# Kernel tuning notes

Measured on AMD Instinct MI355X. Metric: run time of the kernel, lower is better.

## Reference

```python
import jax, jax.numpy as jnp
import numpy as np
import math

E = 8        # num_experts
L2 = 15
L3 = 32
D = 3072     # eval_features_per_perspective
R = 256      # router_features
B = 16384
AUX_ALPHA = 0.01
Z_ALPHA = 0.001


def setup_inputs() -> dict:
    key = jax.random.key(0)
    ks = jax.random.split(key, 12)
    inp = {
        "expert_input": jax.random.uniform(ks[0], (B, D), jnp.float32),
        "router_input": jax.random.normal(ks[1], (R,) , jnp.float32) * 0 + jax.random.normal(ks[1], (B, R), jnp.float32),
        # router init: normal(std=0.01), zero bias (as in _reset_router)
        "router_w": jax.random.normal(ks[2], (E, R), jnp.float32) * 0.01,
        "router_b": jnp.zeros((E,), jnp.float32),
        # FactorizedStackedLinear l1: stacked weight [E*(L2+1), D] + shared factorized [(L2+1), D]
        "l1_w": jax.random.normal(ks[3], (E * (L2 + 1), D), jnp.float32) * (1.0 / math.sqrt(D)),
        "l1_b": jax.random.normal(ks[4], (E * (L2 + 1),), jnp.float32) * 0.01,
        "l1f_w": jax.random.normal(ks[5], (L2 + 1, D), jnp.float32) * (1.0 / math.sqrt(D)),
        "l1f_b": jax.random.normal(ks[6], (L2 + 1,), jnp.float32) * 0.01,
        # StackedLinear l2: [E*L3, 2*L2]
        "l2_w": jax.random.normal(ks[7], (E * L3, 2 * L2), jnp.float32) * (1.0 / math.sqrt(2 * L2)),
        "l2_b": jax.random.normal(ks[8], (E * L3,), jnp.float32) * 0.01,
        # StackedLinear output: [E*1, L3], bias zeroed in __init__
        "out_w": jax.random.normal(ks[9], (E, L3), jnp.float32) * (1.0 / math.sqrt(L3)),
        "out_b": jnp.zeros((E,), jnp.float32),
    }
    return inp


def reference(expert_input, router_input, router_w, router_b,
              l1_w, l1_b, l1f_w, l1f_b, l2_w, l2_b, out_w, out_b):
    # ---- router + straight-through hard gate ----
    gate_logits = router_input @ router_w.T + router_b                      # [B, E]
    gate_probs = jax.nn.softmax(gate_logits, axis=-1)
    expert_indices = jnp.argmax(gate_logits, axis=-1)                       # [B]
    hard_gate = jax.nn.one_hot(expert_indices, E, dtype=gate_probs.dtype)   # [B, E]
    gate = hard_gate + gate_probs - jax.lax.stop_gradient(gate_probs)

    # ---- routing metrics / losses ----
    fraction_routed = hard_gate.mean(axis=0)                                 # [E]
    avg_gate_prob = gate_probs.mean(axis=0)                                  # [E]
    aux_loss = E * jnp.sum(fraction_routed * avg_gate_prob)
    z_loss = jnp.mean(jnp.square(jax.nn.logsumexp(gate_logits, axis=-1)))
    entropy = jnp.mean(-jnp.sum(gate_probs * jnp.log(jnp.clip(gate_probs, 1e-9)), axis=-1))
    normalized_entropy = entropy / jnp.float32(math.log(max(E, 2)))
    top1_prob = jnp.mean(jnp.max(gate_probs, axis=-1))
    router_loss = jnp.float32(AUX_ALPHA) * aux_loss + jnp.float32(Z_ALPHA) * z_loss  # training path

    # ---- l1: FactorizedStackedLinear, dense over all experts (training path) ----
    merged_w = (l1_w + jnp.tile(l1f_w, (E, 1))).reshape(E, L2 + 1, D)        # [E, L2+1, D]
    merged_b = (l1_b + jnp.tile(l1f_b, (E,))).reshape(E, L2 + 1)             # [E, L2+1]
    l1c = jnp.einsum('bi,eoi->beo', expert_input, merged_w) + merged_b[None]  # [B, E, L2+1]
    l1x, l1x_out = l1c[:, :, :L2], l1c[:, :, L2:]                            # [B,E,L2], [B,E,1]
    l1x = jnp.clip(jnp.concatenate([jnp.square(l1x) * (255.0 / 256.0), l1x], axis=2), 0.0, 1.0)  # [B,E,2*L2]

    # ---- l2 + output StackedLinear ----
    w2 = l2_w.reshape(E, L3, 2 * L2)
    l2x = jnp.clip(jnp.einsum('bei,eoi->beo', l1x, w2) + l2_b.reshape(E, L3)[None], 0.0, 1.0)  # [B,E,L3]
    wo = out_w.reshape(E, 1, L3)
    l3x = jnp.einsum('bei,eoi->beo', l2x, wo) + out_b.reshape(E, 1)[None] + l1x_out            # [B,E,1]

    # ---- gated combine ----
    out = jnp.einsum('be,beo->bo', gate, l3x)                                # [B, 1]
    return (out, router_loss, aux_loss, z_loss, fraction_routed, avg_gate_prob,
            normalized_entropy, top1_prob)
```

## Files before the change

kernel.cpp:

```cpp
#include <hip/hip_runtime.h>

constexpr int NB  = 16384;
constexpr int ND  = 3072;
constexpr int NR  = 256;
constexpr int NE  = 8;
constexpr int NO1 = 16;
constexpr int NL2D = 30;
constexpr int NL3 = 32;

constexpr size_t WS_CURSORS = 32;
constexpr size_t WS_OFFPAD  = 128;
constexpr size_t WS_IDX     = 256;
constexpr size_t WS_BUCKET  = WS_IDX + (size_t)NB*4;
constexpr size_t WS_MB      = WS_BUCKET + (size_t)(NB+256)*4;
constexpr size_t WS_MW      = WS_MB + 512;
constexpr size_t WS_BLK_CNT  = WS_MW + (size_t)128*3072*4;
constexpr size_t WS_BLK_SUMP = WS_BLK_CNT + 8192;
constexpr size_t WS_BLK_Z    = WS_BLK_SUMP + 8192;
constexpr size_t WS_BLK_ENT  = WS_BLK_Z + 1024;
constexpr size_t WS_BLK_TOP  = WS_BLK_ENT + 1024;

__device__ __forceinline__ float clamp01(float v) { return fminf(fmaxf(v, 0.0f), 1.0f); }

__device__ __forceinline__ void stage16(const float* g, float* l) {
    __builtin_amdgcn_global_load_lds(
        (const __attribute__((address_space(1))) unsigned int*)g,
        (__attribute__((address_space(3))) unsigned int*)l,
        16, 0, 0);
}

__global__ __launch_bounds__(256) void router_merge_kernel(
    const float* __restrict__ rin, const float* __restrict__ rw,
    const float* __restrict__ rb, int* __restrict__ idx,
    int* __restrict__ blk_cnt, float* __restrict__ blk_sump,
    float* __restrict__ blk_z, float* __restrict__ blk_ent, float* __restrict__ blk_top,
    const float* __restrict__ l1w, const float* __restrict__ l1b,
    const float* __restrict__ l1fw, const float* __restrict__ l1fb,
    float* __restrict__ mw, float* __restrict__ mb)
{
    const int t = threadIdx.x;

    if (blockIdx.x >= 256) {
        const int gid = blockIdx.x - 256;
        const int i4 = gid * 256 + t;
        const float4 a = ((const float4*)l1w)[i4];
        const float4 b = ((const float4*)l1fw)[i4 % (NO1 * ND / 4)];
        float4 r; r.x = a.x + b.x; r.y = a.y + b.y; r.z = a.z + b.z; r.w = a.w + b.w;
        ((float4*)mw)[i4] = r;
        if (gid == 0 && t < NE * NO1) {
            mb[t] = l1b[t] + l1fb[t & (NO1 - 1)];
        }
        return;
    }

    __shared__ float w_s[NE][NR];
    __shared__ float red_f[4][11];
    __shared__ int   red_c[4][8];

    {
        const float4* src = (const float4*)rw;
        float4* dst = (float4*)&w_s[0][0];
        dst[t]       = src[t];
        dst[t + 256] = src[t + 256];
    }
    __syncthreads();

    const int q  = t & 3;
    const int rr = t >> 2;
    const int b  = blockIdx.x * 64 + rr;
    const float* rp = rin + (size_t)b * NR + q * 64;

    float acc[NE];
#pragma unroll
    for (int e = 0; e < NE; ++e) acc[e] = 0.0f;

#pragma unroll
    for (int c = 0; c < 16; ++c) {
        const float4 xv = *(const float4*)(rp + c * 4);
#pragma unroll
        for (int e = 0; e < NE; ++e) {
            const float4 wv = *(const float4*)(&w_s[e][q * 64 + c * 4]);
            acc[e] = fmaf(xv.x, wv.x, acc[e]);
            acc[e] = fmaf(xv.y, wv.y, acc[e]);
            acc[e] = fmaf(xv.z, wv.z, acc[e]);
            acc[e] = fmaf(xv.w, wv.w, acc[e]);
        }
    }
    float lg[NE];
#pragma unroll
    for (int e = 0; e < NE; ++e) {
        float v = acc[e];
        v += __shfl_xor(v, 1);
        v += __shfl_xor(v, 2);
        lg[e] = v + rb[e];
    }

    float m = lg[0]; int am = 0;
#pragma unroll
    for (int e = 1; e < NE; ++e) { if (lg[e] > m) { m = lg[e]; am = e; } }
    float p[NE]; float ssum = 0.0f;
#pragma unroll
    for (int e = 0; e < NE; ++e) { p[e] = __expf(lg[e] - m); ssum += p[e]; }
    const float inv = 1.0f / ssum;
    const float lse = m + __logf(ssum);

    const bool active = (q == 0);
    float sv[11];
    float ent = 0.0f, top = 0.0f;
#pragma unroll
    for (int e = 0; e < NE; ++e) {
        const float pj = p[e] * inv;
        sv[e] = pj;
        ent -= pj * __logf(fmaxf(pj, 1e-9f));
        top = fmaxf(top, pj);
    }
    sv[8] = lse * lse;
    sv[9] = ent;
    sv[10] = top;
    if (!active) {
#pragma unroll
        for (int i = 0; i < 11; ++i) sv[i] = 0.0f;
    }
    if (active) idx[b] = am;

#pragma unroll
    for (int i = 0; i < 11; ++i) {
        float v = sv[i];
        v += __shfl_xor(v, 4);
        v += __shfl_xor(v, 8);
        v += __shfl_xor(v, 16);
        v += __shfl_xor(v, 32);
        sv[i] = v;
    }
    int cnt[NE];
#pragma unroll
    for (int j = 0; j < NE; ++j) {
        unsigned long long mk = __ballot(active && (am == j));
        cnt[j] = __popcll(mk);
    }

    const int wave = t >> 6;
    if ((t & 63) == 0) {
#pragma unroll
        for (int i = 0; i < 11; ++i) red_f[wave][i] = sv[i];
#pragma unroll
        for (int j = 0; j < NE; ++j) red_c[wave][j] = cnt[j];
    }
    __syncthreads();

    const int bid = blockIdx.x;
    if (t < 8) {
        blk_sump[bid * 8 + t] = red_f[0][t] + red_f[1][t] + red_f[2][t] + red_f[3][t];
        blk_cnt [bid * 8 + t] = red_c[0][t] + red_c[1][t] + red_c[2][t] + red_c[3][t];
    } else if (t == 8) {
        blk_z[bid]   = red_f[0][8] + red_f[1][8] + red_f[2][8] + red_f[3][8];
    } else if (t == 9) {
        blk_ent[bid] = red_f[0][9] + red_f[1][9] + red_f[2][9] + red_f[3][9];
    } else if (t == 10) {
        blk_top[bid] = red_f[0][10] + red_f[1][10] + red_f[2][10] + red_f[3][10];
    }
}

__global__ __launch_bounds__(256) void scatter_finalize_kernel(
    const int* __restrict__ blk_cnt, const float* __restrict__ blk_sump,
    const float* __restrict__ blk_z, const float* __restrict__ blk_ent,
    const float* __restrict__ blk_top, const int* __restrict__ idx,
    int* __restrict__ cursors, int* __restrict__ bucket,
    int* __restrict__ offpad, float* __restrict__ out)
{
    const int t = threadIdx.x;

    if (blockIdx.x == 64) {
        __shared__ float ps_s[32][8];
        __shared__ int   pc_s[32][8];
        __shared__ float zet_s[3][4];
        __shared__ float tot_f[8];
        __shared__ int   tot_c[8];
        {
            const int e = t & 7, g = t >> 3;
            float ps = 0.0f; int pc = 0;
#pragma unroll
            for (int k = 0; k < 8; ++k) {
                const int bb = g * 8 + k;
                ps += blk_sump[bb * 8 + e];
                pc += blk_cnt [bb * 8 + e];
            }
            ps_s[g][e] = ps;
            pc_s[g][e] = pc;
        }
        {
            float z = blk_z[t], en = blk_ent[t], tp = blk_top[t];
#pragma unroll
            for (int o = 1; o < 64; o <<= 1) {
                z  += __shfl_xor(z, o);
                en += __shfl_xor(en, o);
                tp += __shfl_xor(tp, o);
            }
            const int wave = t >> 6;
            if ((t & 63) == 0) { zet_s[0][wave] = z; zet_s[1][wave] = en; zet_s[2][wave] = tp; }
        }
        __syncthreads();
        if (t < 8) {
            float s = 0.0f; int c = 0;
            for (int g = 0; g < 32; ++g) { s += ps_s[g][t]; c += pc_s[g][t]; }
            tot_f[t] = s; tot_c[t] = c;
        }
        __syncthreads();
        if (t == 0) {
            int run = 0;
#pragma unroll
            for (int e = 0; e < NE; ++e) {
                offpad[e] = run;
                run += (tot_c[e] + 31) & ~31;
            }
            offpad[NE] = run;

            const float invB = 1.0f / (float)NB;
            float aux = 0.0f;
            float frac[NE], avg[NE];
#pragma unroll
            for (int e = 0; e < NE; ++e) {
                frac[e] = (float)tot_c[e] * invB;
                avg[e]  = tot_f[e] * invB;
                aux += frac[e] * avg[e];
            }
            aux *= (float)NE;
            const float z   = (zet_s[0][0] + zet_s[0][1] + zet_s[0][2] + zet_s[0][3]) * invB;
            const float ent = (zet_s[1][0] + zet_s[1][1] + zet_s[1][2] + zet_s[1][3]) * invB;
            const float top = (zet_s[2][0] + zet_s[2][1] + zet_s[2][2] + zet_s[2][3]) * invB;
            const float rl  = 0.01f * aux + 0.001f * z;

            float* o = out + NB;
            o[0] = rl;
            o[1] = aux;
            o[2] = z;
#pragma unroll
            for (int e = 0; e < NE; ++e) o[3 + e]  = frac[e];
#pragma unroll
            for (int e = 0; e < NE; ++e) o[11 + e] = avg[e];
            o[19] = ent / __logf(8.0f);
            o[20] = top;
        }
        return;
    }

    __shared__ int red_c[4][8];
    __shared__ int offp[8];
    {
        const int4 a = ((const int4*)blk_cnt)[t * 2];
        const int4 bql = ((const int4*)blk_cnt)[t * 2 + 1];
        int v[8] = {a.x, a.y, a.z, a.w, bql.x, bql.y, bql.z, bql.w};
#pragma unroll
        for (int j = 0; j < 8; ++j) {
#pragma unroll
            for (int o = 1; o < 64; o <<= 1) v[j] += __shfl_xor(v[j], o);
        }
        const int wave = t >> 6;
        if ((t & 63) == 0) {
#pragma unroll
            for (int j = 0; j < 8; ++j) red_c[wave][j] = v[j];
        }
    }
    __syncthreads();
    if (t == 0) {
        int run = 0;
#pragma unroll
        for (int e = 0; e < NE; ++e) {
            offp[e] = run;
            run += (red_c[0][e] + red_c[1][e] + red_c[2][e] + red_c[3][e] + 31) & ~31;
        }
    }
    __syncthreads();

    const int b = blockIdx.x * 256 + t;
    const int e = idx[b];
    const int lane = t & 63;
#pragma unroll
    for (int ee = 0; ee < NE; ++ee) {
        unsigned long long mask = __ballot(e == ee);
        if (e == ee) {
            int leader = __ffsll((unsigned long long)mask) - 1;
            int cnt = __popcll(mask);
            int base = 0;
            if (lane == leader) base = atomicAdd(&cursors[ee], cnt);
            base = __shfl(base, leader);
            int pos = base + __popcll(mask & ((1ull << lane) - 1ull));
            bucket[offp[ee] + pos] = b;
        }
    }
}

__global__ __launch_bounds__(256) void moe_main_kernel(
    const float* __restrict__ x, const float* __restrict__ mw,
    const float* __restrict__ mb, const float* __restrict__ l2w,
    const float* __restrict__ l2b, const float* __restrict__ ow,
    const float* __restrict__ ob, const int* __restrict__ bucket,
    const int* __restrict__ offpad, float* __restrict__ out)
{
    __shared__ float x_lds[2][16][128];
    __shared__ float w_lds[2][16][128];
    __shared__ int   rows_s[16];
    __shared__ int   expert_s;
    __shared__ float l1c_s[16][16];
    __shared__ float l1x_s[16][30];
    __shared__ float l1c15_s[16];

    const int t = threadIdx.x;
    const int slot0 = blockIdx.x * 16;
    if (t < 16) rows_s[t] = bucket[slot0 + t];
    if (t == 0) {
        int e = 0;
#pragma unroll
        for (int j = 1; j < NE; ++j) if (slot0 >= offpad[j]) e = j;
        expert_s = e;
    }
    __syncthreads();

    const int e    = expert_s;
    const int wid  = t >> 6;
    const int lane = t & 63;
    const int half = lane >> 5;
    const int s    = lane & 31;

    int srowA = rows_s[4 * wid + half];
    int srowB = rows_s[4 * wid + 2 + half];
    if (srowA < 0) srowA = 0;
    if (srowB < 0) srowB = 0;
    const float* xsrcA = x + (size_t)srowA * ND + s * 4;
    const float* xsrcB = x + (size_t)srowB * ND + s * 4;
    const float* wbase = mw + (size_t)e * NO1 * ND;
    const float* wsrc0 = wbase + (size_t)(4 * wid + 0 + half) * ND + s * 4;
    const float* wsrc1 = wbase + (size_t)(4 * wid + 2 + half) * ND + s * 4;

    float acc[8][4];
#pragma unroll
    for (int rr = 0; rr < 8; ++rr)
#pragma unroll
        for (int oo = 0; oo < 4; ++oo) acc[rr][oo] = 0.0f;

    stage16(xsrcA, &x_lds[0][4 * wid][0]);
    stage16(xsrcB, &x_lds[0][4 * wid + 2][0]);
    stage16(wsrc0, &w_lds[0][4 * wid][0]);
    stage16(wsrc1, &w_lds[0][4 * wid + 2][0]);
    __syncthreads();

    for (int c = 0; c < 24; ++c) {
        const int cur = c & 1;
        const int nxt = cur ^ 1;
        if (c + 1 < 24) {
            const int off = (c + 1) * 128;
            stage16(xsrcA + off, &x_lds[nxt][4 * wid][0]);
            stage16(xsrcB + off, &x_lds[nxt][4 * wid + 2][0]);
            stage16(wsrc0 + off, &w_lds[nxt][4 * wid][0]);
            stage16(wsrc1 + off, &w_lds[nxt][4 * wid + 2][0]);
        }

        float4 wv[4];
#pragma unroll
        for (int oo = 0; oo < 4; ++oo)
            wv[oo] = *(const float4*)&w_lds[cur][4 * wid + oo][s * 4];

#pragma unroll
        for (int rr = 0; rr < 8; ++rr) {
            const float4 xv = *(const float4*)&x_lds[cur][half * 8 + rr][s * 4];
#pragma unroll
            for (int oo = 0; oo < 4; ++oo) {
                float a = acc[rr][oo];
                a = fmaf(xv.x, wv[oo].x, a);
                a = fmaf(xv.y, wv[oo].y, a);
                a = fmaf(xv.z, wv[oo].z, a);
                a = fmaf(xv.w, wv[oo].w, a);
                acc[rr][oo] = a;
            }
        }
        __syncthreads();
    }

#pragma unroll
    for (int rr = 0; rr < 8; ++rr)
#pragma unroll
        for (int oo = 0; oo < 4; ++oo) {
            float a = acc[rr][oo];
            a += __shfl_xor(a, 1);
            a += __shfl_xor(a, 2);
            a += __shfl_xor(a, 4);
            a += __shfl_xor(a, 8);
            a += __shfl_xor(a, 16);
            acc[rr][oo] = a;
        }
    if (s == 0) {
#pragma unroll
        for (int rr = 0; rr < 8; ++rr)
#pragma unroll
            for (int oo = 0; oo < 4; ++oo)
                l1c_s[half * 8 + rr][4 * wid + oo] = acc[rr][oo];
    }
    __syncthreads();

    const int r = t >> 4;
    const int q = t & 15;
    const int rowb = rows_s[r];

    {
        const int o = q;
        float v = l1c_s[r][o] + mb[e * NO1 + o];
        if (o < 15) {
            l1x_s[r][o]      = clamp01(v * v * (255.0f / 256.0f));
            l1x_s[r][o + 15] = clamp01(v);
        } else {
            l1c15_s[r] = v;
        }
    }
    __syncthreads();

    float pacc = 0.0f;
#pragma unroll
    for (int oo = 0; oo < 2; ++oo) {
        const int o2 = q + oo * 16;
        float a2 = l2b[e * NL3 + o2];
        const float* w2r = l2w + (size_t)e * NL3 * NL2D + o2 * NL2D;
#pragma unroll
        for (int i = 0; i < NL2D; ++i) a2 = fmaf(l1x_s[r][i], w2r[i], a2);
        a2 = clamp01(a2);
        pacc = fmaf(a2, ow[e * NL3 + o2], pacc);
    }
    pacc += __shfl_xor(pacc, 1);
    pacc += __shfl_xor(pacc, 2);
    pacc += __shfl_xor(pacc, 4);
    pacc += __shfl_xor(pacc, 8);

    if (q == 0 && rowb >= 0) {
        out[rowb] = pacc + ob[e] + l1c15_s[r];
    }
}

extern "C" void kernel_launch(void* const* d_in, const int* in_sizes, int n_in,
                              void* d_out, int out_size, void* d_ws, size_t ws_size,
                              hipStream_t stream)
{
    const float* x    = (const float*)d_in[0];
    const float* rin  = (const float*)d_in[1];
    const float* rw   = (const float*)d_in[2];
    const float* rb   = (const float*)d_in[3];
    const float* l1w  = (const float*)d_in[4];
    const float* l1b  = (const float*)d_in[5];
    const float* l1fw = (const float*)d_in[6];
    const float* l1fb = (const float*)d_in[7];
    const float* l2w  = (const float*)d_in[8];
    const float* l2b  = (const float*)d_in[9];
    const float* ow   = (const float*)d_in[10];
    const float* ob   = (const float*)d_in[11];
    float* out = (float*)d_out;

    char* ws = (char*)d_ws;
    int*   cursors = (int*)(ws + WS_CURSORS);
    int*   offpad  = (int*)(ws + WS_OFFPAD);
    int*   idx     = (int*)(ws + WS_IDX);
    int*   bucket  = (int*)(ws + WS_BUCKET);
    float* mb      = (float*)(ws + WS_MB);
    float* mw      = (float*)(ws + WS_MW);
    int*   blk_cnt  = (int*)(ws + WS_BLK_CNT);
    float* blk_sump = (float*)(ws + WS_BLK_SUMP);
    float* blk_z    = (float*)(ws + WS_BLK_Z);
    float* blk_ent  = (float*)(ws + WS_BLK_ENT);
    float* blk_top  = (float*)(ws + WS_BLK_TOP);

    hipMemsetAsync(ws, 0, 256, stream);
    hipMemsetAsync(ws + WS_BUCKET, 0xFF, (size_t)(NB + 256) * 4, stream);

    router_merge_kernel<<<640, 256, 0, stream>>>(rin, rw, rb, idx, blk_cnt, blk_sump,
                                                 blk_z, blk_ent, blk_top,
                                                 l1w, l1b, l1fw, l1fb, mw, mb);
    scatter_finalize_kernel<<<65, 256, 0, stream>>>(blk_cnt, blk_sump, blk_z, blk_ent,
                                                    blk_top, idx, cursors, bucket,
                                                    offpad, out);
    moe_main_kernel<<<(NB + 256) / 16, 256, 0, stream>>>(x, mw, mb, l2w, l2b, ow, ob,
                                                         bucket, offpad, out);
}
```

Baseline: 115.2 us.

## Replace LDS-staged l1 GEMM with register-direct loads, 4 rows x 16 outputs per wave

The main MoE kernel's first-layer dot products no longer stage x and merged weights through double-buffered LDS with async global-to-LDS copies and per-chunk barriers. Each wave now loads its 4 token rows straight into registers with register double-buffering, reads all 16 weight rows directly from global memory (expected to hit in cache since every block of an expert shares them), and accumulates 4x16 outputs per lane. The goal is to remove LDS traffic and the block-wide syncs from the inner loop. In exchange the accumulator count per thread grows, the cross-lane reduction gets one extra shuffle step, and weight reads now depend on cache hits instead of explicit reuse in LDS.

```diff
diff --git a/kernel.cpp b/kernel.cpp
--- a/kernel.cpp
+++ b/kernel.cpp
@@ -22,13 +22,6 @@
 
 __device__ __forceinline__ float clamp01(float v) { return fminf(fmaxf(v, 0.0f), 1.0f); }
 
-__device__ __forceinline__ void stage16(const float* g, float* l) {
-    __builtin_amdgcn_global_load_lds(
-        (const __attribute__((address_space(1))) unsigned int*)g,
-        (__attribute__((address_space(3))) unsigned int*)l,
-        16, 0, 0);
-}
-
 __global__ __launch_bounds__(256) void router_merge_kernel(
     const float* __restrict__ rin, const float* __restrict__ rw,
     const float* __restrict__ rb, int* __restrict__ idx,
@@ -297,8 +290,6 @@
     const float* __restrict__ ob, const int* __restrict__ bucket,
     const int* __restrict__ offpad, float* __restrict__ out)
 {
-    __shared__ float x_lds[2][16][128];
-    __shared__ float w_lds[2][16][128];
     __shared__ int   rows_s[16];
     __shared__ int   expert_s;
     __shared__ float l1c_s[16][16];
@@ -319,81 +310,72 @@
     const int e    = expert_s;
     const int wid  = t >> 6;
     const int lane = t & 63;
-    const int half = lane >> 5;
-    const int s    = lane & 31;
-
-    int srowA = rows_s[4 * wid + half];
-    int srowB = rows_s[4 * wid + 2 + half];
-    if (srowA < 0) srowA = 0;
-    if (srowB < 0) srowB = 0;
-    const float* xsrcA = x + (size_t)srowA * ND + s * 4;
-    const float* xsrcB = x + (size_t)srowB * ND + s * 4;
-    const float* wbase = mw + (size_t)e * NO1 * ND;
-    const float* wsrc0 = wbase + (size_t)(4 * wid + 0 + half) * ND + s * 4;
-    const float* wsrc1 = wbase + (size_t)(4 * wid + 2 + half) * ND + s * 4;
-
-    float acc[8][4];
-#pragma unroll
-    for (int rr = 0; rr < 8; ++rr)
-#pragma unroll
-        for (int oo = 0; oo < 4; ++oo) acc[rr][oo] = 0.0f;
-
-    stage16(xsrcA, &x_lds[0][4 * wid][0]);
-    stage16(xsrcB, &x_lds[0][4 * wid + 2][0]);
-    stage16(wsrc0, &w_lds[0][4 * wid][0]);
-    stage16(wsrc1, &w_lds[0][4 * wid + 2][0]);
-    __syncthreads();
-
-    for (int c = 0; c < 24; ++c) {
-        const int cur = c & 1;
-        const int nxt = cur ^ 1;
-        if (c + 1 < 24) {
-            const int off = (c + 1) * 128;
-            stage16(xsrcA + off, &x_lds[nxt][4 * wid][0]);
-            stage16(xsrcB + off, &x_lds[nxt][4 * wid + 2][0]);
-            stage16(wsrc0 + off, &w_lds[nxt][4 * wid][0]);
-            stage16(wsrc1 + off, &w_lds[nxt][4 * wid + 2][0]);
-        }
-
-        float4 wv[4];
-#pragma unroll
-        for (int oo = 0; oo < 4; ++oo)
-            wv[oo] = *(const float4*)&w_lds[cur][4 * wid + oo][s * 4];
-
-#pragma unroll
-        for (int rr = 0; rr < 8; ++rr) {
-            const float4 xv = *(const float4*)&x_lds[cur][half * 8 + rr][s * 4];
-#pragma unroll
-            for (int oo = 0; oo < 4; ++oo) {
-                float a = acc[rr][oo];
-                a = fmaf(xv.x, wv[oo].x, a);
-                a = fmaf(xv.y, wv[oo].y, a);
-                a = fmaf(xv.z, wv[oo].z, a);
-                a = fmaf(xv.w, wv[oo].w, a);
-                acc[rr][oo] = a;
+
+    const float* xsrc[4];
+#pragma unroll
+    for (int rr = 0; rr < 4; ++rr) {
+        int r = rows_s[4 * wid + rr];
+        if (r < 0) r = 0;
+        xsrc[rr] = x + (size_t)r * ND + lane * 4;
+    }
+    const float* wbase = mw + (size_t)e * NO1 * ND + lane * 4;
+
+    float acc[4][16];
+#pragma unroll
+    for (int rr = 0; rr < 4; ++rr)
+#pragma unroll
+        for (int o = 0; o < 16; ++o) acc[rr][o] = 0.0f;
+
+    float4 xcur[4], xnxt[4];
+#pragma unroll
+    for (int rr = 0; rr < 4; ++rr) xcur[rr] = *(const float4*)(xsrc[rr]);
+#pragma unroll
+    for (int rr = 0; rr < 4; ++rr) xnxt[rr] = xcur[rr];
+
+    for (int c = 0; c < 12; ++c) {
+        if (c + 1 < 12) {
+#pragma unroll
+            for (int rr = 0; rr < 4; ++rr)
+                xnxt[rr] = *(const float4*)(xsrc[rr] + (c + 1) * 256);
+        }
+
+        const float* wk = wbase + c * 256;
+#pragma unroll
+        for (int o = 0; o < 16; ++o) {
+            const float4 wv = *(const float4*)(wk + (size_t)o * ND);
+#pragma unroll
+            for (int rr = 0; rr < 4; ++rr) {
+                float a = acc[rr][o];
+                a = fmaf(xcur[rr].x, wv.x, a);
+                a = fmaf(xcur[rr].y, wv.y, a);
+                a = fmaf(xcur[rr].z, wv.z, a);
+                a = fmaf(xcur[rr].w, wv.w, a);
+                acc[rr][o] = a;
             }
         }
-        __syncthreads();
-    }
-
-#pragma unroll
-    for (int rr = 0; rr < 8; ++rr)
-#pragma unroll
-        for (int oo = 0; oo < 4; ++oo) {
-            float a = acc[rr][oo];
+#pragma unroll
+        for (int rr = 0; rr < 4; ++rr) xcur[rr] = xnxt[rr];
+    }
+
+#pragma unroll
+    for (int rr = 0; rr < 4; ++rr)
+#pragma unroll
+        for (int o = 0; o < 16; ++o) {
+            float a = acc[rr][o];
             a += __shfl_xor(a, 1);
             a += __shfl_xor(a, 2);
             a += __shfl_xor(a, 4);
             a += __shfl_xor(a, 8);
             a += __shfl_xor(a, 16);
-            acc[rr][oo] = a;
-        }
-    if (s == 0) {
-#pragma unroll
-        for (int rr = 0; rr < 8; ++rr)
-#pragma unroll
-            for (int oo = 0; oo < 4; ++oo)
-                l1c_s[half * 8 + rr][4 * wid + oo] = acc[rr][oo];
+            a += __shfl_xor(a, 32);
+            acc[rr][o] = a;
+        }
+    if (lane == 0) {
+#pragma unroll
+        for (int rr = 0; rr < 4; ++rr)
+#pragma unroll
+            for (int o = 0; o < 16; ++o)
+                l1c_s[4 * wid + rr][o] = acc[rr][o];
     }
     __syncthreads();
 
```

New measurement: 113.1 us. No clear change (-1.9%).
